# Optimization experiments

Hardware: AMD Instinct MI355X
Metric: run time of the kernel (lower is better)

The kernel has to match this reference:

```python
import jax, jax.numpy as jnp
import numpy as np
from jax import lax

B, T, EPROJS, DUNITS, ATT_DIM = 32, 2048, 1024, 1024, 512
ACONV_CHANS, ACONV_FILTS = 32, 15
SCALING = 2.0


def setup_inputs() -> dict:
    key = jax.random.key(0)
    ks = jax.random.split(key, 12)
    enc_hs_pad = jax.random.normal(ks[0], (B, T, EPROJS), dtype=jnp.float32)
    enc_hs_len = jax.random.randint(ks[1], (B,), T // 2, T + 1, dtype=jnp.int32)
    dec_z = jax.random.normal(ks[2], (B, DUNITS), dtype=jnp.float32)
    ap = jax.random.uniform(ks[3], (B, T), dtype=jnp.float32)
    att_prev = ap / jnp.sum(ap, axis=1, keepdims=True)  # previous attention distribution
    # parameters (PyTorch Linear: y = x @ W^T + b; stored here pre-transposed as [in, out])
    s_enc = 1.0 / np.sqrt(EPROJS)
    s_dec = 1.0 / np.sqrt(DUNITS)
    s_att = 1.0 / np.sqrt(ACONV_CHANS)
    s_g = 1.0 / np.sqrt(ATT_DIM)
    K = 2 * ACONV_FILTS + 1
    s_c = 1.0 / np.sqrt(K)
    W_enc = jax.random.uniform(ks[4], (EPROJS, ATT_DIM), jnp.float32, -s_enc, s_enc)
    b_enc = jax.random.uniform(ks[5], (ATT_DIM,), jnp.float32, -s_enc, s_enc)
    W_dec = jax.random.uniform(ks[6], (DUNITS, ATT_DIM), jnp.float32, -s_dec, s_dec)
    W_att = jax.random.uniform(ks[7], (ACONV_CHANS, ATT_DIM), jnp.float32, -s_att, s_att)
    conv_w = jax.random.uniform(ks[8], (ACONV_CHANS, 1, K), jnp.float32, -s_c, s_c)
    W_g = jax.random.uniform(ks[9], (ATT_DIM, 1), jnp.float32, -s_g, s_g)
    b_g = jax.random.uniform(ks[10], (1,), jnp.float32, -s_g, s_g)
    return {"enc_hs_pad": enc_hs_pad, "enc_hs_len": enc_hs_len, "dec_z": dec_z,
            "att_prev": att_prev, "W_enc": W_enc, "b_enc": b_enc, "W_dec": W_dec,
            "W_att": W_att, "conv_w": conv_w, "W_g": W_g, "b_g": b_g}


def reference(enc_hs_pad, enc_hs_len, dec_z, att_prev,
              W_enc, b_enc, W_dec, W_att, conv_w, W_g, b_g):
    # pre-computed encoder projection: (B, T, A)
    pre_enc = jnp.einsum('btd,da->bta', enc_hs_pad, W_enc) + b_enc
    # location conv over previous attention: (B, 1, T) -> (B, C, T), SAME padding
    pad = (conv_w.shape[-1] - 1) // 2
    att_conv = lax.conv_general_dilated(
        att_prev[:, None, :], conv_w, window_strides=(1,),
        padding=[(pad, pad)], dimension_numbers=('NCH', 'OIH', 'NCH'))
    att_c = jnp.einsum('bct,ca->bta', att_conv, W_att)       # (B, T, A)
    dec_t = (dec_z @ W_dec)[:, None, :]                       # (B, 1, A)
    # energies: (B, T)
    e = jnp.einsum('bta,ao->bt', jnp.tanh(att_c + pre_enc + dec_t), W_g) + b_g[0]
    # pad mask: True where t >= length
    mask = jnp.arange(e.shape[1])[None, :] >= enc_hs_len[:, None]
    e = jnp.where(mask, -jnp.inf, e)
    w = jax.nn.softmax(SCALING * e, axis=1)                   # (B, T)
    c = jnp.einsum('btd,bt->bd', enc_hs_pad, w)               # (B, EPROJS)
    return c, w
```

## Files before the change

### kernel.cpp

```cpp
#include <hip/hip_runtime.h>
#include <stdint.h>

#define T_LEN 2048
#define KAUG  1056
#define M_TOT 65536

typedef __attribute__((ext_vector_type(8))) short short8;
typedef __attribute__((ext_vector_type(4))) float f32x4;
typedef unsigned int u32;
typedef unsigned short u16;

__device__ __forceinline__ u16 bf16_rn(float f){
  u32 u = __builtin_bit_cast(u32, f);
  u32 r = u + 0x7fffu + ((u >> 16) & 1u);
  return (u16)(r >> 16);
}
__device__ __forceinline__ u32 pack_trunc(float lo, float hi){
  u32 a = __builtin_bit_cast(u32, lo);
  u32 b = __builtin_bit_cast(u32, hi);
  return (a >> 16) | (b & 0xffff0000u);
}
__device__ __forceinline__ void lds_load16(const void* g, void* l){
  __builtin_amdgcn_global_load_lds(
      (const __attribute__((address_space(1))) u32*)g,
      (__attribute__((address_space(3))) u32*)l, 16, 0, 0);
}

__global__ void k_build_bt(const float* __restrict__ W_enc,
                           const float* __restrict__ W_att,
                           u16* __restrict__ Bt){
  __shared__ float tile[32][33];
  int k0 = blockIdx.x * 32, n0 = blockIdx.y * 32;
  int tx = threadIdx.x & 31, ty = threadIdx.x >> 5;
  #pragma unroll
  for (int i = 0; i < 4; i++){
    int k = k0 + i*8 + ty;
    int n = n0 + tx;
    float v = (k < 1024) ? W_enc[k*512 + n] : W_att[(k-1024)*512 + n];
    tile[i*8+ty][tx] = v;
  }
  __syncthreads();
  #pragma unroll
  for (int i = 0; i < 4; i++){
    int n = n0 + i*8 + ty;
    int k = k0 + tx;
    Bt[(size_t)n*KAUG + k] = bf16_rn(tile[tx][i*8+ty]);
  }
}

__global__ void k_bias(const float* __restrict__ dec_z,
                       const float* __restrict__ W_dec,
                       const float* __restrict__ b_enc,
                       float* __restrict__ bias){
  __shared__ float red[4][64];
  int b = blockIdx.y, n0 = blockIdx.x * 64;
  int nl = threadIdx.x & 63, ks = threadIdx.x >> 6;
  int n = n0 + nl;
  const float* dz = dec_z + b*1024;
  float s = 0.f;
  #pragma unroll 4
  for (int k = ks*256; k < ks*256 + 256; k++) s += dz[k] * W_dec[k*512 + n];
  red[ks][nl] = s;
  __syncthreads();
  if (threadIdx.x < 64){
    int nn = n0 + threadIdx.x;
    bias[b*512 + nn] = b_enc[nn] + red[0][threadIdx.x] + red[1][threadIdx.x]
                     + red[2][threadIdx.x] + red[3][threadIdx.x];
  }
}

__global__ void k_conv(const float* __restrict__ att_prev,
                       const float* __restrict__ conv_w,
                       float* __restrict__ attT){
  int idx = blockIdx.x*256 + threadIdx.x;
  int c = idx & 31;
  int bt = idx >> 5;
  int b = bt >> 11, t = bt & 2047;
  const float* ap = att_prev + b*2048;
  const float* cw = conv_w + c*31;
  float s = 0.f;
  #pragma unroll
  for (int j = 0; j < 31; j++){
    int tt = t + j - 15;
    float a = (tt >= 0 && tt < 2048) ? ap[tt] : 0.f;
    s += cw[j] * a;
  }
  attT[(size_t)bt*32 + c] = s;
}

__launch_bounds__(256)
__global__ void k_gemm_energy(const float* __restrict__ enc,
                              const float* __restrict__ attT,
                              const u16* __restrict__ Bt,
                              const float* __restrict__ bias,
                              const float* __restrict__ Wg,
                              float* __restrict__ ePart){
  __shared__ float Ash[128*32];
  __shared__ u16   Bsh[128*32];
  __shared__ float eRed[2][128];

  const int tid  = threadIdx.x;
  const int lane = tid & 63;
  const int wid  = tid >> 6;
  const int wave_m = wid >> 1, wave_n = wid & 1;
  const int bidx = blockIdx.x;
  const int xcd  = bidx & 7;
  const int s_sq = bidx >> 3;
  const int nblk = s_sq & 3;
  const int mblk = ((s_sq >> 2) << 3) + xcd;
  const int row0 = mblk << 7;
  const int b    = mblk >> 4;

  f32x4 acc[4][4];
  #pragma unroll
  for (int i = 0; i < 4; i++)
    #pragma unroll
    for (int j = 0; j < 4; j++) acc[i][j] = (f32x4)(0.f);

  const int arow_in = lane >> 3;
  const int ap_phys = lane & 7;
  const int brow_in = lane >> 2;
  const int bp_phys = lane & 3;
  const int fr_m = lane & 15;
  const int kg   = lane >> 4;

  const u16* BtN = Bt + (size_t)(nblk*128)*KAUG;

  #pragma unroll 1
  for (int kk = 0; kk < 33; ++kk){
    const float* srcA; int rstr;
    if (kk < 32){ srcA = enc  + (size_t)row0*1024 + kk*32; rstr = 1024; }
    else        { srcA = attT + (size_t)row0*32;           rstr = 32;   }
    #pragma unroll
    for (int q = 0; q < 4; q++){
      int r = wid*32 + q*8 + arow_in;
      int c = ap_phys ^ (r & 7);
      lds_load16(srcA + (size_t)r*rstr + c*4, Ash + (wid*32 + q*8)*32);
    }
    const u16* srcB = BtN + kk*32;
    #pragma unroll
    for (int q = 0; q < 2; q++){
      int n = wid*32 + q*16 + brow_in;
      int c = bp_phys ^ ((n >> 1) & 3);
      lds_load16(srcB + (size_t)n*KAUG + c*8, Bsh + (wid*32 + q*16)*32);
    }
    __syncthreads();

    short8 afrag[4], bfrag[4];
    #pragma unroll
    for (int mi = 0; mi < 4; mi++){
      int m  = wave_m*64 + mi*16 + fr_m;
      int c0 = kg*2;
      int p0 = c0 ^ (m & 7), p1 = (c0+1) ^ (m & 7);
      const f32x4* rowp = (const f32x4*)(Ash + m*32);
      f32x4 x0 = rowp[p0];
      f32x4 x1 = rowp[p1];
      union { u32 u[4]; short8 s; } cv;
      cv.u[0] = pack_trunc(x0.x, x0.y);
      cv.u[1] = pack_trunc(x0.z, x0.w);
      cv.u[2] = pack_trunc(x1.x, x1.y);
      cv.u[3] = pack_trunc(x1.z, x1.w);
      afrag[mi] = cv.s;
    }
    #pragma unroll
    for (int ni = 0; ni < 4; ni++){
      int n = wave_n*64 + ni*16 + fr_m;
      int p = kg ^ ((n >> 1) & 3);
      bfrag[ni] = *(const short8*)(Bsh + n*32 + p*8);
    }
    #pragma unroll
    for (int mi = 0; mi < 4; mi++)
      #pragma unroll
      for (int ni = 0; ni < 4; ni++)
        acc[mi][ni] = __builtin_amdgcn_mfma_f32_16x16x32_bf16(afrag[mi], bfrag[ni], acc[mi][ni], 0, 0, 0);

    __syncthreads();
  }

  float wg[4], bs[4];
  #pragma unroll
  for (int ni = 0; ni < 4; ni++){
    int ng = nblk*128 + wave_n*64 + ni*16 + fr_m;
    wg[ni] = Wg[ng];
    bs[ni] = bias[b*512 + ng];
  }
  #pragma unroll
  for (int mi = 0; mi < 4; mi++){
    #pragma unroll
    for (int reg = 0; reg < 4; reg++){
      float s = 0.f;
      #pragma unroll
      for (int ni = 0; ni < 4; ni++){
        float v  = acc[mi][ni][reg] + bs[ni];
        float e2 = __expf(2.f * v);
        float th = 1.f - 2.f/(e2 + 1.f);
        s += wg[ni] * th;
      }
      s += __shfl_xor(s, 1);
      s += __shfl_xor(s, 2);
      s += __shfl_xor(s, 4);
      s += __shfl_xor(s, 8);
      if (fr_m == 0){
        int rowl = wave_m*64 + mi*16 + kg*4 + reg;
        eRed[wave_n][rowl] = s;
      }
    }
  }
  __syncthreads();
  if (tid < 128)
    ePart[(size_t)nblk*M_TOT + row0 + tid] = eRed[0][tid] + eRed[1][tid];
}

__global__ void k_softmax(const float* __restrict__ ePart,
                          const int* __restrict__ lens,
                          float* __restrict__ wout){
  int b = blockIdx.x, tid = threadIdx.x;
  int lane = tid & 63, wid = tid >> 6;
  int len = lens[b];
  __shared__ float red[4];
  float x[8]; float m = -3.0e38f;
  #pragma unroll
  for (int i = 0; i < 8; i++){
    int t = tid + i*256;
    int idx = b*2048 + t;
    float e = ePart[idx] + ePart[M_TOT + idx] + ePart[2*M_TOT + idx] + ePart[3*M_TOT + idx];
    float xx = (t < len) ? 2.0f*e : -3.0e38f;
    x[i] = xx; m = fmaxf(m, xx);
  }
  #pragma unroll
  for (int o = 1; o < 64; o <<= 1) m = fmaxf(m, __shfl_xor(m, o));
  if (lane == 0) red[wid] = m;
  __syncthreads();
  m = fmaxf(fmaxf(red[0], red[1]), fmaxf(red[2], red[3]));
  float s = 0.f;
  #pragma unroll
  for (int i = 0; i < 8; i++){
    float ex = (x[i] > -1.0e38f) ? __expf(x[i] - m) : 0.f;
    x[i] = ex; s += ex;
  }
  #pragma unroll
  for (int o = 1; o < 64; o <<= 1) s += __shfl_xor(s, o);
  __syncthreads();
  if (lane == 0) red[wid] = s;
  __syncthreads();
  s = red[0] + red[1] + red[2] + red[3];
  float inv = 1.0f / s;
  #pragma unroll
  for (int i = 0; i < 8; i++){
    int t = tid + i*256;
    wout[b*2048 + t] = x[i]*inv;
  }
}

__global__ void k_ctx_partial(const float* __restrict__ enc,
                              const float* __restrict__ w,
                              float* __restrict__ cPart){
  int dc = blockIdx.x, tc = blockIdx.y, b = blockIdx.z;
  int d = dc*256 + threadIdx.x;
  const float* ep = enc + ((size_t)(b*2048 + tc*256))*1024 + d;
  const float* wp = w + b*2048 + tc*256;
  float s0 = 0, s1 = 0, s2 = 0, s3 = 0;
  #pragma unroll 2
  for (int t = 0; t < 256; t += 4){
    s0 += wp[t+0] * ep[(size_t)(t+0)*1024];
    s1 += wp[t+1] * ep[(size_t)(t+1)*1024];
    s2 += wp[t+2] * ep[(size_t)(t+2)*1024];
    s3 += wp[t+3] * ep[(size_t)(t+3)*1024];
  }
  cPart[((size_t)tc*32 + b)*1024 + d] = (s0 + s1) + (s2 + s3);
}

__global__ void k_ctx_reduce(const float* __restrict__ cPart, float* __restrict__ cOut){
  int idx = blockIdx.x*256 + threadIdx.x;
  float s = 0.f;
  #pragma unroll
  for (int tc = 0; tc < 8; tc++) s += cPart[tc*32768 + idx];
  cOut[idx] = s;
}

extern "C" void kernel_launch(void* const* d_in, const int* in_sizes, int n_in,
                              void* d_out, int out_size, void* d_ws, size_t ws_size,
                              hipStream_t stream){
  (void)in_sizes; (void)n_in; (void)out_size; (void)ws_size;
  const float* enc    = (const float*)d_in[0];
  const int*   lens   = (const int*)  d_in[1];
  const float* dec_z  = (const float*)d_in[2];
  const float* att_p  = (const float*)d_in[3];
  const float* W_enc  = (const float*)d_in[4];
  const float* b_enc  = (const float*)d_in[5];
  const float* W_dec  = (const float*)d_in[6];
  const float* W_att  = (const float*)d_in[7];
  const float* conv_w = (const float*)d_in[8];
  const float* W_g    = (const float*)d_in[9];

  char* ws = (char*)d_ws;
  u16*   Bt    = (u16*)  (ws);
  float* attT  = (float*)(ws + 1081344);
  float* bias  = (float*)(ws + 1081344 + 8388608);
  float* ePart = (float*)(ws + 1081344 + 8388608 + 65536);
  float* cPart = (float*)(ws + 1081344 + 8388608 + 65536 + 1048576);

  float* c_out = (float*)d_out;
  float* w_out = c_out + 32*1024;

  hipLaunchKernelGGL(k_build_bt,    dim3(33,16),  dim3(256), 0, stream, W_enc, W_att, Bt);
  hipLaunchKernelGGL(k_bias,        dim3(8,32),   dim3(256), 0, stream, dec_z, W_dec, b_enc, bias);
  hipLaunchKernelGGL(k_conv,        dim3(8192),   dim3(256), 0, stream, att_p, conv_w, attT);
  hipLaunchKernelGGL(k_gemm_energy, dim3(2048),   dim3(256), 0, stream, enc, attT, Bt, bias, W_g, ePart);
  hipLaunchKernelGGL(k_softmax,     dim3(32),     dim3(256), 0, stream, ePart, lens, w_out);
  hipLaunchKernelGGL(k_ctx_partial, dim3(4,8,32), dim3(256), 0, stream, enc, w_out, cPart);
  hipLaunchKernelGGL(k_ctx_reduce,  dim3(128),    dim3(256), 0, stream, cPart, c_out);
}
```

Measured before the change: 594.1 us.

## Triple-buffer LDS tiles in energy GEMM to overlap loads with MFMA

Replaces the single-buffered K loop in the energy GEMM with a three-stage LDS ring. Tiles are prefetched two iterations ahead via global_load_lds, and explicit vmcnt waits plus raw barriers replace __syncthreads. The goal is to hide global memory latency behind MFMA work. In exchange LDS use per block triples, which may lower occupancy, and correctness relies on hand-counted vmcnt values matching the six loads issued per stage.

```diff
diff --git a/kernel.cpp b/kernel.cpp
--- a/kernel.cpp
+++ b/kernel.cpp
@@ -95,8 +95,8 @@
                               const float* __restrict__ bias,
                               const float* __restrict__ Wg,
                               float* __restrict__ ePart){
-  __shared__ float Ash[128*32];
-  __shared__ u16   Bsh[128*32];
+  __shared__ float Ash[3][128*32];
+  __shared__ u16   Bsh[3][128*32];
   __shared__ float eRed[2][128];
 
   const int tid  = threadIdx.x;
@@ -126,25 +126,46 @@
 
   const u16* BtN = Bt + (size_t)(nblk*128)*KAUG;
 
-  #pragma unroll 1
-  for (int kk = 0; kk < 33; ++kk){
+  auto STAGE = [&](int t, int bufi){
     const float* srcA; int rstr;
-    if (kk < 32){ srcA = enc  + (size_t)row0*1024 + kk*32; rstr = 1024; }
-    else        { srcA = attT + (size_t)row0*32;           rstr = 32;   }
+    if (t < 32){ srcA = enc  + (size_t)row0*1024 + t*32; rstr = 1024; }
+    else       { srcA = attT + (size_t)row0*32;          rstr = 32;   }
+    float* ab = &Ash[bufi][0];
     #pragma unroll
     for (int q = 0; q < 4; q++){
       int r = wid*32 + q*8 + arow_in;
       int c = ap_phys ^ (r & 7);
-      lds_load16(srcA + (size_t)r*rstr + c*4, Ash + (wid*32 + q*8)*32);
-    }
-    const u16* srcB = BtN + kk*32;
+      lds_load16(srcA + (size_t)r*rstr + c*4, ab + (wid*32 + q*8)*32);
+    }
+    const u16* srcB = BtN + t*32;
+    u16* bb = &Bsh[bufi][0];
     #pragma unroll
     for (int q = 0; q < 2; q++){
       int n = wid*32 + q*16 + brow_in;
       int c = bp_phys ^ ((n >> 1) & 3);
-      lds_load16(srcB + (size_t)n*KAUG + c*8, Bsh + (wid*32 + q*16)*32);
-    }
-    __syncthreads();
+      lds_load16(srcB + (size_t)n*KAUG + c*8, bb + (wid*32 + q*16)*32);
+    }
+  };
+
+  STAGE(0, 0);
+  STAGE(1, 1);
+
+  int cur = 0, stg = 2;
+  #pragma unroll 1
+  for (int kk = 0; kk < 33; ++kk){
+    if (kk < 31){
+      STAGE(kk + 2, stg);
+      asm volatile("s_waitcnt vmcnt(12)" ::: "memory");
+    } else if (kk == 31){
+      asm volatile("s_waitcnt vmcnt(6)" ::: "memory");
+    } else {
+      asm volatile("s_waitcnt vmcnt(0)" ::: "memory");
+    }
+    __builtin_amdgcn_s_barrier();
+    asm volatile("" ::: "memory");
+
+    const float* Abuf = &Ash[cur][0];
+    const u16*   Bbuf = &Bsh[cur][0];
 
     short8 afrag[4], bfrag[4];
     #pragma unroll
@@ -152,7 +173,7 @@
       int m  = wave_m*64 + mi*16 + fr_m;
       int c0 = kg*2;
       int p0 = c0 ^ (m & 7), p1 = (c0+1) ^ (m & 7);
-      const f32x4* rowp = (const f32x4*)(Ash + m*32);
+      const f32x4* rowp = (const f32x4*)(Abuf + m*32);
       f32x4 x0 = rowp[p0];
       f32x4 x1 = rowp[p1];
       union { u32 u[4]; short8 s; } cv;
@@ -166,7 +187,7 @@
     for (int ni = 0; ni < 4; ni++){
       int n = wave_n*64 + ni*16 + fr_m;
       int p = kg ^ ((n >> 1) & 3);
-      bfrag[ni] = *(const short8*)(Bsh + n*32 + p*8);
+      bfrag[ni] = *(const short8*)(Bbuf + n*32 + p*8);
     }
     #pragma unroll
     for (int mi = 0; mi < 4; mi++)
@@ -174,7 +195,10 @@
       for (int ni = 0; ni < 4; ni++)
         acc[mi][ni] = __builtin_amdgcn_mfma_f32_16x16x32_bf16(afrag[mi], bfrag[ni], acc[mi][ni], 0, 0, 0);
 
-    __syncthreads();
+    asm volatile("" ::: "memory");
+    __builtin_amdgcn_s_barrier();
+    cur = (cur == 2) ? 0 : cur + 1;
+    stg = (stg == 2) ? 0 : stg + 1;
   }
 
   float wg[4], bs[4];
```

New measurement: 628.4 us. 5.8% more time.

## Register-prefetch double-buffered GEMM with bf16 LDS staging and direct B fragment loads

Applied to the files above, without the earlier changes.

Replaces the single-buffered global_load_lds pipeline with a register-prefetch scheme. The next A tile is loaded into registers and converted to bf16 before it is written into one of two LDS buffers, while B fragments are read straight from global memory into registers. Each k-step needs one barrier instead of two, and the LDS footprint roughly halves, which together with launch_bounds(256,3) aims for higher occupancy. In exchange it raises register pressure, and the B fragment loads from global memory may be less coalesced because each lane reads 16 bytes from a different row.

```diff
diff --git a/kernel.cpp b/kernel.cpp
--- a/kernel.cpp
+++ b/kernel.cpp
@@ -19,11 +19,6 @@
   u32 a = __builtin_bit_cast(u32, lo);
   u32 b = __builtin_bit_cast(u32, hi);
   return (a >> 16) | (b & 0xffff0000u);
-}
-__device__ __forceinline__ void lds_load16(const void* g, void* l){
-  __builtin_amdgcn_global_load_lds(
-      (const __attribute__((address_space(1))) u32*)g,
-      (__attribute__((address_space(3))) u32*)l, 16, 0, 0);
 }
 
 __global__ void k_build_bt(const float* __restrict__ W_enc,
@@ -88,15 +83,14 @@
   attT[(size_t)bt*32 + c] = s;
 }
 
-__launch_bounds__(256)
+__launch_bounds__(256, 3)
 __global__ void k_gemm_energy(const float* __restrict__ enc,
                               const float* __restrict__ attT,
                               const u16* __restrict__ Bt,
                               const float* __restrict__ bias,
                               const float* __restrict__ Wg,
                               float* __restrict__ ePart){
-  __shared__ float Ash[128*32];
-  __shared__ u16   Bsh[128*32];
+  __shared__ __align__(16) u16 Ash[2][128*32];
   __shared__ float eRed[2][128];
 
   const int tid  = threadIdx.x;
@@ -117,65 +111,95 @@
     #pragma unroll
     for (int j = 0; j < 4; j++) acc[i][j] = (f32x4)(0.f);
 
-  const int arow_in = lane >> 3;
-  const int ap_phys = lane & 7;
-  const int brow_in = lane >> 2;
-  const int bp_phys = lane & 3;
+  const int srow = lane >> 2;
+  const int sc   = lane & 3;
   const int fr_m = lane & 15;
   const int kg   = lane >> 4;
 
   const u16* BtN = Bt + (size_t)(nblk*128)*KAUG;
 
-  #pragma unroll 1
-  for (int kk = 0; kk < 33; ++kk){
-    const float* srcA; int rstr;
-    if (kk < 32){ srcA = enc  + (size_t)row0*1024 + kk*32; rstr = 1024; }
-    else        { srcA = attT + (size_t)row0*32;           rstr = 32;   }
-    #pragma unroll
-    for (int q = 0; q < 4; q++){
-      int r = wid*32 + q*8 + arow_in;
-      int c = ap_phys ^ (r & 7);
-      lds_load16(srcA + (size_t)r*rstr + c*4, Ash + (wid*32 + q*8)*32);
+  int r0q[2], ldsoff[2];
+  #pragma unroll
+  for (int q = 0; q < 2; q++){
+    int r = wid*32 + q*16 + srow;
+    r0q[q] = r;
+    ldsoff[q] = r*32 + (sc ^ ((r >> 1) & 3))*8;
+  }
+  int aroff[4];
+  #pragma unroll
+  for (int mi = 0; mi < 4; mi++){
+    int m = wave_m*64 + mi*16 + fr_m;
+    aroff[mi] = m*32 + (kg ^ ((m >> 1) & 3))*8;
+  }
+  int bnrow[4];
+  #pragma unroll
+  for (int ni = 0; ni < 4; ni++)
+    bnrow[ni] = wave_n*64 + ni*16 + fr_m;
+
+  auto LOADA = [&](int t, f32x4* ra){
+    const float* base; size_t rstr;
+    if (t < 32){ base = enc + (size_t)row0*1024 + t*32; rstr = 1024; }
+    else       { base = attT + (size_t)row0*32;         rstr = 32;  }
+    #pragma unroll
+    for (int q = 0; q < 2; q++){
+      const float* p = base + (size_t)r0q[q]*rstr + sc*8;
+      ra[q*2+0] = *(const f32x4*)(p);
+      ra[q*2+1] = *(const f32x4*)(p + 4);
     }
-    const u16* srcB = BtN + kk*32;
+  };
+  auto LOADBF = [&](int t, short8* bf){
+    #pragma unroll
+    for (int ni = 0; ni < 4; ni++)
+      bf[ni] = *(const short8*)(BtN + (size_t)bnrow[ni]*KAUG + t*32 + kg*8);
+  };
+  auto WRITEA = [&](const f32x4* ra, int bi){
     #pragma unroll
     for (int q = 0; q < 2; q++){
-      int n = wid*32 + q*16 + brow_in;
-      int c = bp_phys ^ ((n >> 1) & 3);
-      lds_load16(srcB + (size_t)n*KAUG + c*8, Bsh + (wid*32 + q*16)*32);
+      f32x4 lo = ra[q*2+0], hi = ra[q*2+1];
+      union { u32 u[4]; short8 v; } cv;
+      cv.u[0] = pack_trunc(lo.x, lo.y);
+      cv.u[1] = pack_trunc(lo.z, lo.w);
+      cv.u[2] = pack_trunc(hi.x, hi.y);
+      cv.u[3] = pack_trunc(hi.z, hi.w);
+      *(short8*)&Ash[bi][ldsoff[q]] = cv.v;
     }
-    __syncthreads();
-
-    short8 afrag[4], bfrag[4];
+  };
+  auto COMPUTE = [&](int bi, const short8* bf){
+    const u16* Ab = &Ash[bi][0];
     #pragma unroll
     for (int mi = 0; mi < 4; mi++){
-      int m  = wave_m*64 + mi*16 + fr_m;
-      int c0 = kg*2;
-      int p0 = c0 ^ (m & 7), p1 = (c0+1) ^ (m & 7);
-      const f32x4* rowp = (const f32x4*)(Ash + m*32);
-      f32x4 x0 = rowp[p0];
-      f32x4 x1 = rowp[p1];
-      union { u32 u[4]; short8 s; } cv;
-      cv.u[0] = pack_trunc(x0.x, x0.y);
-      cv.u[1] = pack_trunc(x0.z, x0.w);
-      cv.u[2] = pack_trunc(x1.x, x1.y);
-      cv.u[3] = pack_trunc(x1.z, x1.w);
-      afrag[mi] = cv.s;
-    }
-    #pragma unroll
-    for (int ni = 0; ni < 4; ni++){
-      int n = wave_n*64 + ni*16 + fr_m;
-      int p = kg ^ ((n >> 1) & 3);
-      bfrag[ni] = *(const short8*)(Bsh + n*32 + p*8);
-    }
-    #pragma unroll
-    for (int mi = 0; mi < 4; mi++)
+      short8 af = *(const short8*)(Ab + aroff[mi]);
       #pragma unroll
       for (int ni = 0; ni < 4; ni++)
-        acc[mi][ni] = __builtin_amdgcn_mfma_f32_16x16x32_bf16(afrag[mi], bfrag[ni], acc[mi][ni], 0, 0, 0);
-
-    __syncthreads();
-  }
+        acc[mi][ni] = __builtin_amdgcn_mfma_f32_16x16x32_bf16(af, bf[ni], acc[mi][ni], 0, 0, 0);
+    }
+  };
+
+  f32x4 raA[4], raB[4];
+  short8 bfA[4], bfB[4];
+  LOADA(0, raA); LOADBF(0, bfA);
+
+  #pragma unroll 1
+  for (int i = 0; i < 16; i++){
+    int kk = 2*i;
+    LOADA(kk+1, raB); LOADBF(kk+1, bfB);
+    WRITEA(raA, 0);
+    asm volatile("s_waitcnt lgkmcnt(0)" ::: "memory");
+    __builtin_amdgcn_s_barrier();
+    asm volatile("" ::: "memory");
+    COMPUTE(0, bfA);
+    LOADA(kk+2, raA); LOADBF(kk+2, bfA);
+    WRITEA(raB, 1);
+    asm volatile("s_waitcnt lgkmcnt(0)" ::: "memory");
+    __builtin_amdgcn_s_barrier();
+    asm volatile("" ::: "memory");
+    COMPUTE(1, bfB);
+  }
+  WRITEA(raA, 0);
+  asm volatile("s_waitcnt lgkmcnt(0)" ::: "memory");
+  __builtin_amdgcn_s_barrier();
+  asm volatile("" ::: "memory");
+  COMPUTE(0, bfA);
 
   float wg[4], bs[4];
   #pragma unroll
```

New measurement: 601.9 us. No clear change (+1.3%).
